# Performance work log

Hardware: AMD Instinct MI355X
Metric: run time of the kernel (lower is better)

Reference implementation:

```python
import jax, jax.numpy as jnp
import numpy as np

PAD, BOS, EOS = 0, 1, 2
VOCAB, EMB, HID, N, T = 32, 32, 512, 4096, 64


def _lstm_step(x, h, c, W_ih, W_hh, b_ih, b_hh):
    # PyTorch nn.LSTM single step; gate order [i|f|g|o]
    g = x @ W_ih.T + h @ W_hh.T + b_ih + b_hh  # [n, 4H]
    i, f, gg, o = jnp.split(g, 4, axis=-1)
    i = jax.nn.sigmoid(i)
    f = jax.nn.sigmoid(f)
    gg = jnp.tanh(gg)
    o = jax.nn.sigmoid(o)
    c = f * c + i * gg
    h = o * jnp.tanh(c)
    return h, c


def setup_inputs() -> dict:
    key = jax.random.key(0)
    ks = jax.random.split(key, 12)
    s = 0.04  # ~1/sqrt(hidden), matches torch LSTM init scale
    emb = jax.random.normal(ks[0], (VOCAB, EMB), jnp.float32) * s
    emb = emb.at[PAD].set(0.0)  # padding_idx row is zero
    inp = {
        "prevs": jnp.full((N, 1), BOS, dtype=jnp.int32),
        "emb": emb,
        "W_ih0": jax.random.normal(ks[1], (4 * HID, EMB), jnp.float32) * s,
        "W_hh0": jax.random.normal(ks[2], (4 * HID, HID), jnp.float32) * s,
        "b_ih0": jax.random.normal(ks[3], (4 * HID,), jnp.float32) * s,
        "b_hh0": jax.random.normal(ks[4], (4 * HID,), jnp.float32) * s,
        "W_ih1": jax.random.normal(ks[5], (4 * HID, HID), jnp.float32) * s,
        "W_hh1": jax.random.normal(ks[6], (4 * HID, HID), jnp.float32) * s,
        "b_ih1": jax.random.normal(ks[7], (4 * HID,), jnp.float32) * s,
        "b_hh1": jax.random.normal(ks[8], (4 * HID,), jnp.float32) * s,
        "W_out": jax.random.normal(ks[9], (VOCAB, HID), jnp.float32) * s,
        "b_out": jax.random.normal(ks[10], (VOCAB,), jnp.float32) * s,
        "max_length": T,
    }
    return inp


def reference(prevs, emb, W_ih0, W_hh0, b_ih0, b_hh0,
              W_ih1, W_hh1, b_ih1, b_hh1, W_out, b_out, max_length):
    # softmax+multinomial sampling, <eos>/<pad> bookkeeping.
    n = prevs.shape[0]
    H = W_hh0.shape[1]
    keys = jax.random.split(jax.random.key(7), max_length)
    tok0 = prevs[:, 0]
    h0 = jnp.zeros((n, H), emb.dtype)
    init = (tok0, h0, h0, h0, h0,
            tok0 == EOS, jnp.zeros((n,), jnp.int32))

    def step(carry, key):
        tok, h0, c0, h1, c1, is_end, lengths = carry
        x = emb[tok]                                   # [n, EMB]
        h0, c0 = _lstm_step(x, h0, c0, W_ih0, W_hh0, b_ih0, b_hh0)
        h1, c1 = _lstm_step(h0, h1, c1, W_ih1, W_hh1, b_ih1, b_hh1)
        logits = h1 @ W_out.T + b_out                  # [n, VOCAB]
        sampled = jax.random.categorical(key, logits)  # == multinomial(softmax)
        cur = jnp.where(is_end, PAD, sampled).astype(tok.dtype)
        lengths = lengths + (~is_end).astype(jnp.int32)
        is_end = is_end | (cur == EOS)
        return (cur, h0, c0, h1, c1, is_end, lengths), cur

    carry, toks = jax.lax.scan(step, init, keys)       # toks: [T, n]
    lengths = carry[-1] + 1                            # +1 for <bos>
    samples = jnp.concatenate([prevs, toks.T], axis=1)  # [n, 1+T]
    return samples, lengths
```

## Files before the change

kernel.cpp:

```cpp
#include <hip/hip_runtime.h>
#include <cstdint>
#include <cmath>

#define RNG_VARIANT 1

#define NROWS 4096
#define HIDN 512
#define VOC 32
#define TSTEPS 64
#define PAD_TOK 0
#define BOS_TOK 1
#define EOS_TOK 2

#define BK 32
#define BM 128
#define JJT 32

typedef const __attribute__((address_space(1))) unsigned int* gptr_t;
typedef __attribute__((address_space(3))) unsigned int* lptr_t;

__host__ __device__ inline void tf2x32(unsigned k0, unsigned k1, unsigned x0, unsigned x1,
                                       unsigned& o0, unsigned& o1) {
  unsigned ks0 = k0, ks1 = k1, ks2 = k0 ^ k1 ^ 0x1BD11BDAu;
  unsigned X0 = x0 + ks0, X1 = x1 + ks1;
  const unsigned R[5][4] = {{13,15,26,6},{17,29,16,24},{13,15,26,6},{17,29,16,24},{13,15,26,6}};
  unsigned inj0[5], inj1[5];
  inj0[0] = ks1; inj1[0] = ks2;
  inj0[1] = ks2; inj1[1] = ks0;
  inj0[2] = ks0; inj1[2] = ks1;
  inj0[3] = ks1; inj1[3] = ks2;
  inj0[4] = ks2; inj1[4] = ks0;
#pragma unroll
  for (int i = 0; i < 5; ++i) {
#pragma unroll
    for (int j = 0; j < 4; ++j) {
      X0 += X1;
      unsigned r = R[i][j];
      X1 = (X1 << r) | (X1 >> (32 - r));
      X1 ^= X0;
    }
    X0 += inj0[i];
    X1 += inj1[i] + (unsigned)(i + 1);
  }
  o0 = X0; o1 = X1;
}

template<int NPARTS, bool LAYER0>
__global__ __launch_bounds__(256, 2) void lstm_fused(
    const float* __restrict__ A0, const float* __restrict__ B0,
    const float* __restrict__ A1, const float* __restrict__ B1,
    const float* __restrict__ extra,
    const int* __restrict__ tokv,
    float* __restrict__ h, float* __restrict__ c)
{
  __shared__ float As[2][BM * BK];
  __shared__ float Bs[2][BM * BK];
  const int tid = threadIdx.x;
  const int lane = tid & 63;
  const int w = tid >> 6;
  const int wr = w >> 1, wc = w & 1;
  const int ty = lane >> 3, tx = lane & 7;
  const int m0 = blockIdx.y * BM;
  const int c0 = blockIdx.x * JJT;

  float acc[8][8];
#pragma unroll
  for (int i = 0; i < 8; ++i)
#pragma unroll
    for (int j = 0; j < 8; ++j) acc[i][j] = 0.f;

  const int NT = NPARTS * (HIDN / BK);
  const int g8 = lane >> 3;
  const int ch = lane & 7;

  auto STAGE = [&](int tt, int sel) {
    const float* A = A0;
    const float* B = B0;
    if (NPARTS == 2 && (tt >> 4)) { A = A1; B = B1; }
    const int kb = (tt & 15) * BK;
    float* dA = &As[sel][0];
    float* dB = &Bs[sel][0];
#pragma unroll
    for (int i = 0; i < 4; ++i) {
      const int rbase = w * 32 + i * 8;
      const int swz = (rbase >> 3) & 7;
      const int mA = rbase + g8;
      const float* sA = A + (size_t)(m0 + mA) * HIDN + kb + ((ch ^ swz) << 2);
      __builtin_amdgcn_global_load_lds((gptr_t)sA, (lptr_t)(dA + rbase * BK), 16, 0, 0);
      const int mB = rbase + g8;
      const int grB = (mB & 3) * HIDN + c0 + (mB >> 2);
      const float* sB = B + (size_t)grB * HIDN + kb + ((ch ^ swz) << 2);
      __builtin_amdgcn_global_load_lds((gptr_t)sB, (lptr_t)(dB + rbase * BK), 16, 0, 0);
    }
  };

  STAGE(0, 0);
  __syncthreads();
  int sel = 0;
  const int aRow = wr * 64 + ty * 8;
  const int bRow = wc * 64 + tx * 8;
  for (int tt = 0; tt < NT; ++tt) {
    if (tt + 1 < NT) STAGE(tt + 1, sel ^ 1);
    const float* As_ = &As[sel][0];
    const float* Bs_ = &Bs[sel][0];
#pragma unroll
    for (int kg = 0; kg < 8; ++kg) {
      float4 av[8], bv[8];
#pragma unroll
      for (int i = 0; i < 8; ++i)
        av[i] = *(const float4*)(As_ + (aRow + i) * BK + ((kg ^ ty) << 2));
#pragma unroll
      for (int j = 0; j < 8; ++j)
        bv[j] = *(const float4*)(Bs_ + (bRow + j) * BK + ((kg ^ tx) << 2));
#pragma unroll
      for (int i = 0; i < 8; ++i)
#pragma unroll
        for (int j = 0; j < 8; ++j)
          acc[i][j] = fmaf(av[i].x, bv[j].x, acc[i][j]);
#pragma unroll
      for (int i = 0; i < 8; ++i)
#pragma unroll
        for (int j = 0; j < 8; ++j)
          acc[i][j] = fmaf(av[i].y, bv[j].y, acc[i][j]);
#pragma unroll
      for (int i = 0; i < 8; ++i)
#pragma unroll
        for (int j = 0; j < 8; ++j)
          acc[i][j] = fmaf(av[i].z, bv[j].z, acc[i][j]);
#pragma unroll
      for (int i = 0; i < 8; ++i)
#pragma unroll
        for (int j = 0; j < 8; ++j)
          acc[i][j] = fmaf(av[i].w, bv[j].w, acc[i][j]);
    }
    __syncthreads();
    sel ^= 1;
  }

  const int jjl = wc * 16 + tx * 2;
  const size_t colb = (size_t)(c0 + jjl);
  float e[8];
  if (!LAYER0) {
    float4 e0 = *(const float4*)(extra + colb * 4);
    float4 e1 = *(const float4*)(extra + colb * 4 + 4);
    e[0] = e0.x; e[1] = e0.y; e[2] = e0.z; e[3] = e0.w;
    e[4] = e1.x; e[5] = e1.y; e[6] = e1.z; e[7] = e1.w;
  }
#pragma unroll
  for (int i = 0; i < 8; ++i) {
    const int n = m0 + wr * 64 + ty * 8 + i;
    if (LAYER0) {
      const int tk = tokv[n];
      const float* ex = extra + (size_t)tk * 2048 + colb * 4;
      float4 e0 = *(const float4*)(ex);
      float4 e1 = *(const float4*)(ex + 4);
      e[0] = e0.x; e[1] = e0.y; e[2] = e0.z; e[3] = e0.w;
      e[4] = e1.x; e[5] = e1.y; e[6] = e1.z; e[7] = e1.w;
    }
    float gi0 = acc[i][0] + e[0], gf0 = acc[i][1] + e[1];
    float gg0 = acc[i][2] + e[2], go0 = acc[i][3] + e[3];
    float gi1 = acc[i][4] + e[4], gf1 = acc[i][5] + e[5];
    float gg1 = acc[i][6] + e[6], go1 = acc[i][7] + e[7];
    const size_t idx = (size_t)n * HIDN + colb;
    float2 cold = *(const float2*)(c + idx);
    float si0 = 1.f / (1.f + expf(-gi0));
    float sf0 = 1.f / (1.f + expf(-gf0));
    float tg0 = tanhf(gg0);
    float so0 = 1.f / (1.f + expf(-go0));
    float cn0 = sf0 * cold.x + si0 * tg0;
    float hn0 = so0 * tanhf(cn0);
    float si1 = 1.f / (1.f + expf(-gi1));
    float sf1 = 1.f / (1.f + expf(-gf1));
    float tg1 = tanhf(gg1);
    float so1 = 1.f / (1.f + expf(-go1));
    float cn1 = sf1 * cold.y + si1 * tg1;
    float hn1 = so1 * tanhf(cn1);
    *(float2*)(c + idx) = make_float2(cn0, cn1);
    *(float2*)(h + idx) = make_float2(hn0, hn1);
  }
}

__global__ void build_ew0(const float* __restrict__ emb, const float* __restrict__ W_ih0,
                          const float* __restrict__ b_ih0, const float* __restrict__ b_hh0,
                          float* __restrict__ EW0i)
{
  int idx = blockIdx.x * 256 + threadIdx.x;
  int vv = idx >> 11, j = idx & 2047;
  float s = b_ih0[j] + b_hh0[j];
#pragma unroll
  for (int e = 0; e < 32; ++e)
    s = fmaf(emb[vv * 32 + e], W_ih0[(size_t)j * 32 + e], s);
  EW0i[(size_t)vv * 2048 + (size_t)(j & 511) * 4 + (j >> 9)] = s;
}

__global__ void build_bias1i(const float* __restrict__ a, const float* __restrict__ b,
                             float* __restrict__ o) {
  int j = blockIdx.x * 256 + threadIdx.x;
  o[(size_t)(j & 511) * 4 + (j >> 9)] = a[j] + b[j];
}

__global__ void init_state(const int* __restrict__ prevs, int* __restrict__ tok,
                           int* __restrict__ is_end, int* __restrict__ lengths,
                           int* __restrict__ out)
{
  int n = blockIdx.x * 256 + threadIdx.x;
  if (n < NROWS) {
    int p = prevs[n];
    tok[n] = p;
    is_end[n] = (p == EOS_TOK) ? 1 : 0;
    lengths[n] = 0;
    out[(size_t)n * (TSTEPS + 1)] = p;
  }
}

__global__ __launch_bounds__(64) void sample_step(
    const float* __restrict__ h1, const float* __restrict__ W_out,
    const float* __restrict__ b_out,
    int* __restrict__ tok, int* __restrict__ is_end, int* __restrict__ lengths,
    int* __restrict__ out, unsigned key0, unsigned key1, int t, int last)
{
  __shared__ float hrow[HIDN];
  const int n = blockIdx.x;
  const int lane = threadIdx.x;
  {
    const float4* src = reinterpret_cast<const float4*>(h1 + (size_t)n * HIDN);
    float4* dst = reinterpret_cast<float4*>(hrow);
    dst[lane] = src[lane];
    dst[lane + 64] = src[lane + 64];
  }
  __syncthreads();
  const int v = lane & 31, half = lane >> 5;
  const float* wp = W_out + (size_t)v * HIDN + half * 256;
  const float* hh = hrow + half * 256;
  float dot = 0.f;
#pragma unroll
  for (int k = 0; k < 256; k += 4) {
    float4 wv = *reinterpret_cast<const float4*>(wp + k);
    float4 hv = *reinterpret_cast<const float4*>(hh + k);
    dot = fmaf(wv.x, hv.x, dot);
    dot = fmaf(wv.y, hv.y, dot);
    dot = fmaf(wv.z, hv.z, dot);
    dot = fmaf(wv.w, hv.w, dot);
  }
  dot += __shfl_xor(dot, 32);
  const float logit = dot + b_out[v];

  const unsigned iflat = (unsigned)(n * 32 + v);
  unsigned r0, r1, bits;
#if RNG_VARIANT == 1
  tf2x32(key0, key1, 0u, iflat, r0, r1);
  bits = r0 ^ r1;
#elif RNG_VARIANT == 2
  if (iflat < 65536u) { tf2x32(key0, key1, iflat, iflat + 65536u, r0, r1); bits = r0; }
  else                { tf2x32(key0, key1, iflat - 65536u, iflat, r0, r1); bits = r1; }
#else
  tf2x32(key0, key1, 0u, iflat, r0, r1);
  bits = r1;
#endif
  float f = __uint_as_float((bits >> 9) | 0x3f800000u) - 1.0f;
  float u = fmaxf(f, 1.1754943508222875e-38f);
  float t1 = -(float)log((double)u);
  float g  = -(float)log((double)t1);
  float s = g + logit;

  float bs = s; int bi = v;
#pragma unroll
  for (int off = 16; off >= 1; off >>= 1) {
    float os = __shfl_xor(bs, off);
    int   oi = __shfl_xor(bi, off);
    if (os > bs || (os == bs && oi < bi)) { bs = os; bi = oi; }
  }
  if (lane == 0) {
    const int oe  = is_end[n];
    const int cur = oe ? PAD_TOK : bi;
    const int len = lengths[n] + (oe ? 0 : 1);
    lengths[n] = len;
    is_end[n] = (oe || (cur == EOS_TOK)) ? 1 : 0;
    tok[n] = cur;
    out[(size_t)n * (TSTEPS + 1) + t + 1] = cur;
    if (last) out[(size_t)NROWS * (TSTEPS + 1) + n] = len + 1;
  }
}

extern "C" void kernel_launch(void* const* d_in, const int* in_sizes, int n_in,
                              void* d_out, int out_size, void* d_ws, size_t ws_size,
                              hipStream_t stream)
{
  const int*   prevs = (const int*)d_in[0];
  const float* emb   = (const float*)d_in[1];
  const float* W_ih0 = (const float*)d_in[2];
  const float* W_hh0 = (const float*)d_in[3];
  const float* b_ih0 = (const float*)d_in[4];
  const float* b_hh0 = (const float*)d_in[5];
  const float* W_ih1 = (const float*)d_in[6];
  const float* W_hh1 = (const float*)d_in[7];
  const float* b_ih1 = (const float*)d_in[8];
  const float* b_hh1 = (const float*)d_in[9];
  const float* W_out = (const float*)d_in[10];
  const float* b_out = (const float*)d_in[11];

  const size_t S = (size_t)NROWS * HIDN;
  float* h0a   = (float*)d_ws;
  float* h1a   = h0a + S;
  float* cl0   = h1a + S;
  float* cl1   = cl0 + S;
  float* h0b   = cl1 + S;
  float* h1b   = h0b + S;
  float* EW0i  = h1b + S;
  float* bias1i = EW0i + (size_t)VOC * 2048;
  int* tok     = (int*)(bias1i + 2048);
  int* is_end  = tok + NROWS;
  int* lengths = is_end + NROWS;
  int* outp    = (int*)d_out;

  hipMemsetAsync(h0a, 0, 4 * S * sizeof(float), stream);
  init_state<<<NROWS / 256, 256, 0, stream>>>(prevs, tok, is_end, lengths, outp);
  build_ew0<<<VOC * 2048 / 256, 256, 0, stream>>>(emb, W_ih0, b_ih0, b_hh0, EW0i);
  build_bias1i<<<2048 / 256, 256, 0, stream>>>(b_ih1, b_hh1, bias1i);

  unsigned keys[TSTEPS][2];
  for (int t = 0; t < TSTEPS; ++t) {
    unsigned o0, o1;
    tf2x32(0u, 7u, 0u, (unsigned)t, o0, o1);
    keys[t][0] = o0; keys[t][1] = o1;
  }

  dim3 ggrid(HIDN / JJT, NROWS / BM);
  for (int t = 0; t < TSTEPS; ++t) {
    float* h0rd = (t & 1) ? h0b : h0a;
    float* h0wr = (t & 1) ? h0a : h0b;
    float* h1rd = (t & 1) ? h1b : h1a;
    float* h1wr = (t & 1) ? h1a : h1b;
    lstm_fused<1, true><<<ggrid, 256, 0, stream>>>(
        h0rd, W_hh0, nullptr, nullptr, EW0i, tok, h0wr, cl0);
    lstm_fused<2, false><<<ggrid, 256, 0, stream>>>(
        h0wr, W_ih1, h1rd, W_hh1, bias1i, nullptr, h1wr, cl1);
    sample_step<<<NROWS, 64, 0, stream>>>(h1wr, W_out, b_out, tok, is_end, lengths, outp,
                                          keys[t][0], keys[t][1], t, t == TSTEPS - 1);
  }
}
```

Baseline: 25.44 ms.

## Compact active rows per step and skip finished sequences in LSTM and sampling

Sequences that have emitted EOS are recorded in a per-step list of active row indices, built with atomic appends in the sampling kernel. The fused LSTM GEMM kernels gather A rows through this list and exit early for row tiles beyond the active count. The sampler also exits early for inactive slots, and a separate kernel writes final lengths. The output is pre-zeroed so finished rows yield PAD. This avoids gate GEMMs and sampling for dead sequences, at the cost of gathered row loads, atomics and a nondeterministic row order within tiles.

```diff
diff --git a/kernel.cpp b/kernel.cpp
--- a/kernel.cpp
+++ b/kernel.cpp
@@ -51,8 +51,13 @@
     const float* __restrict__ A1, const float* __restrict__ B1,
     const float* __restrict__ extra,
     const int* __restrict__ tokv,
+    const int* __restrict__ list, const int* __restrict__ cnt, int t,
     float* __restrict__ h, float* __restrict__ c)
 {
+  const int nact = cnt[t];
+  const int m0 = blockIdx.y * BM;
+  if (m0 >= nact) return;
+
   __shared__ float As[2][BM * BK];
   __shared__ float Bs[2][BM * BK];
   const int tid = threadIdx.x;
@@ -60,18 +65,26 @@
   const int w = tid >> 6;
   const int wr = w >> 1, wc = w & 1;
   const int ty = lane >> 3, tx = lane & 7;
-  const int m0 = blockIdx.y * BM;
   const int c0 = blockIdx.x * JJT;
-
-  float acc[8][8];
-#pragma unroll
-  for (int i = 0; i < 8; ++i)
-#pragma unroll
-    for (int j = 0; j < 8; ++j) acc[i][j] = 0.f;
-
-  const int NT = NPARTS * (HIDN / BK);
+  const int toff = t * NROWS;
+
   const int g8 = lane >> 3;
   const int ch = lane & 7;
+
+  int ra[4];
+#pragma unroll
+  for (int i = 0; i < 4; ++i) {
+    const int slot = m0 + w * 32 + i * 8 + g8;
+    ra[i] = (slot < nact) ? list[toff + slot] : 0;
+  }
+
+  float acc[8][8];
+#pragma unroll
+  for (int i = 0; i < 8; ++i)
+#pragma unroll
+    for (int j = 0; j < 8; ++j) acc[i][j] = 0.f;
+
+  const int NT = NPARTS * (HIDN / BK);
 
   auto STAGE = [&](int tt, int sel) {
     const float* A = A0;
@@ -84,8 +97,7 @@
     for (int i = 0; i < 4; ++i) {
       const int rbase = w * 32 + i * 8;
       const int swz = (rbase >> 3) & 7;
-      const int mA = rbase + g8;
-      const float* sA = A + (size_t)(m0 + mA) * HIDN + kb + ((ch ^ swz) << 2);
+      const float* sA = A + (size_t)ra[i] * HIDN + kb + ((ch ^ swz) << 2);
       __builtin_amdgcn_global_load_lds((gptr_t)sA, (lptr_t)(dA + rbase * BK), 16, 0, 0);
       const int mB = rbase + g8;
       const int grB = (mB & 3) * HIDN + c0 + (mB >> 2);
@@ -148,7 +160,9 @@
   }
 #pragma unroll
   for (int i = 0; i < 8; ++i) {
-    const int n = m0 + wr * 64 + ty * 8 + i;
+    const int slot = m0 + wr * 64 + ty * 8 + i;
+    if (slot >= nact) continue;
+    const int n = list[toff + slot];
     if (LAYER0) {
       const int tk = tokv[n];
       const float* ex = extra + (size_t)tk * 2048 + colb * 4;
@@ -200,27 +214,35 @@
 }
 
 __global__ void init_state(const int* __restrict__ prevs, int* __restrict__ tok,
-                           int* __restrict__ is_end, int* __restrict__ lengths,
-                           int* __restrict__ out)
+                           int* __restrict__ lengths, int* __restrict__ out,
+                           int* __restrict__ list, int* __restrict__ cnt)
 {
   int n = blockIdx.x * 256 + threadIdx.x;
   if (n < NROWS) {
     int p = prevs[n];
     tok[n] = p;
-    is_end[n] = (p == EOS_TOK) ? 1 : 0;
     lengths[n] = 0;
     out[(size_t)n * (TSTEPS + 1)] = p;
+    if (p != EOS_TOK) {
+      int pos = atomicAdd(&cnt[0], 1);
+      list[pos] = n;
+    }
   }
 }
 
 __global__ __launch_bounds__(64) void sample_step(
     const float* __restrict__ h1, const float* __restrict__ W_out,
     const float* __restrict__ b_out,
-    int* __restrict__ tok, int* __restrict__ is_end, int* __restrict__ lengths,
-    int* __restrict__ out, unsigned key0, unsigned key1, int t, int last)
-{
+    int* __restrict__ tok, int* __restrict__ lengths,
+    int* __restrict__ out, int* __restrict__ list, int* __restrict__ cnt,
+    unsigned key0, unsigned key1, int t)
+{
+  const int nact = cnt[t];
+  const int b = blockIdx.x;
+  if (b >= nact) return;
+  const int n = list[t * NROWS + b];
+
   __shared__ float hrow[HIDN];
-  const int n = blockIdx.x;
   const int lane = threadIdx.x;
   {
     const float4* src = reinterpret_cast<const float4*>(h1 + (size_t)n * HIDN);
@@ -271,15 +293,21 @@
     if (os > bs || (os == bs && oi < bi)) { bs = os; bi = oi; }
   }
   if (lane == 0) {
-    const int oe  = is_end[n];
-    const int cur = oe ? PAD_TOK : bi;
-    const int len = lengths[n] + (oe ? 0 : 1);
-    lengths[n] = len;
-    is_end[n] = (oe || (cur == EOS_TOK)) ? 1 : 0;
+    const int cur = bi;
+    lengths[n] = lengths[n] + 1;
     tok[n] = cur;
     out[(size_t)n * (TSTEPS + 1) + t + 1] = cur;
-    if (last) out[(size_t)NROWS * (TSTEPS + 1) + n] = len + 1;
-  }
+    if (cur != EOS_TOK) {
+      int pos = atomicAdd(&cnt[t + 1], 1);
+      list[(t + 1) * NROWS + pos] = n;
+    }
+  }
+}
+
+__global__ void final_lengths(const int* __restrict__ lengths, int* __restrict__ out)
+{
+  int n = blockIdx.x * 256 + threadIdx.x;
+  if (n < NROWS) out[(size_t)NROWS * (TSTEPS + 1) + n] = lengths[n] + 1;
 }
 
 extern "C" void kernel_launch(void* const* d_in, const int* in_sizes, int n_in,
@@ -309,12 +337,15 @@
   float* EW0i  = h1b + S;
   float* bias1i = EW0i + (size_t)VOC * 2048;
   int* tok     = (int*)(bias1i + 2048);
-  int* is_end  = tok + NROWS;
-  int* lengths = is_end + NROWS;
+  int* lengths = tok + NROWS;
+  int* list    = lengths + NROWS;
+  int* cnt     = list + (TSTEPS + 1) * NROWS;
   int* outp    = (int*)d_out;
 
   hipMemsetAsync(h0a, 0, 4 * S * sizeof(float), stream);
-  init_state<<<NROWS / 256, 256, 0, stream>>>(prevs, tok, is_end, lengths, outp);
+  hipMemsetAsync(cnt, 0, (TSTEPS + 1) * sizeof(int), stream);
+  hipMemsetAsync(outp, 0, (size_t)out_size * sizeof(int), stream);
+  init_state<<<NROWS / 256, 256, 0, stream>>>(prevs, tok, lengths, outp, list, cnt);
   build_ew0<<<VOC * 2048 / 256, 256, 0, stream>>>(emb, W_ih0, b_ih0, b_hh0, EW0i);
   build_bias1i<<<2048 / 256, 256, 0, stream>>>(b_ih1, b_hh1, bias1i);
 
@@ -332,10 +363,11 @@
     float* h1rd = (t & 1) ? h1b : h1a;
     float* h1wr = (t & 1) ? h1a : h1b;
     lstm_fused<1, true><<<ggrid, 256, 0, stream>>>(
-        h0rd, W_hh0, nullptr, nullptr, EW0i, tok, h0wr, cl0);
+        h0rd, W_hh0, nullptr, nullptr, EW0i, tok, list, cnt, t, h0wr, cl0);
     lstm_fused<2, false><<<ggrid, 256, 0, stream>>>(
-        h0wr, W_ih1, h1rd, W_hh1, bias1i, nullptr, h1wr, cl1);
-    sample_step<<<NROWS, 64, 0, stream>>>(h1wr, W_out, b_out, tok, is_end, lengths, outp,
-                                          keys[t][0], keys[t][1], t, t == TSTEPS - 1);
-  }
-}
+        h0wr, W_ih1, h1rd, W_hh1, bias1i, nullptr, list, cnt, t, h1wr, cl1);
+    sample_step<<<NROWS, 64, 0, stream>>>(h1wr, W_out, b_out, tok, lengths, outp,
+                                          list, cnt, keys[t][0], keys[t][1], t);
+  }
+  final_lengths<<<NROWS / 256, 256, 0, stream>>>(lengths, outp);
+}
```

After: 21.32 ms. 1.19x faster.
